# Optimization experiments

Hardware: AMD Instinct MI355X
Metric: run time of the kernel (lower is better)

The kernel has to match this reference:

```python
import jax, jax.numpy as jnp
import numpy as np

ALPHA = 0.2  # LeakyReLU negative slope
NEG_INF = -9e15


def setup_inputs() -> dict:
    key = jax.random.key(0)
    k1, k2, k3, k4 = jax.random.split(key, 4)
    B, N, F_IN, F_OUT = 2, 4096, 128, 64
    h = jax.random.normal(k1, (B, N, F_IN), dtype=jnp.float32)
    adj = jax.random.randint(k2, (N, N), 0, 2, dtype=jnp.int32)
    W = jax.random.normal(k3, (F_IN, F_OUT), dtype=jnp.float32) * (1.414 / np.sqrt(F_IN))
    a = jax.random.normal(k4, (2 * F_OUT, 1), dtype=jnp.float32) * 0.1
    return {"h": h, "adj": adj, "W": W, "a": a}


def reference(h, adj, W, a):
    # h: (B, N, F_in), adj: (N, N), W: (F_in, F_out), a: (2*F_out, 1)
    Wh = jnp.einsum("bnf,fo->bno", h, W)  # (B, N, F_out)
    F_out = W.shape[1]
    a1 = a[:F_out, 0]   # attends to source node i
    a2 = a[F_out:, 0]   # attends to target node j
    # e_ij = leakyrelu(a1.Wh_i + a2.Wh_j)  -- rank-1 decomposition of the
    # original cat([Wh_i, Wh_j]) @ a, identical math without O(N^2*2F) tensor.
    s1 = Wh @ a1  # (B, N)
    s2 = Wh @ a2  # (B, N)
    e = s1[:, :, None] + s2[:, None, :]  # (B, N, N)
    e = jnp.where(e >= 0, e, ALPHA * e)  # LeakyReLU
    scores = jnp.where(adj[None, :, :] > 0, e, NEG_INF)
    attention = jax.nn.softmax(scores, axis=-1)
    # dropout=0 (eval/deterministic baseline)
    h_prime = jnp.einsum("bij,bjo->bio", attention, Wh)  # (B, N, F_out)
    return jax.nn.elu(h_prime)  # concat=True branch
```

## Files before the change

### kernel.cpp

```cpp
#include <hip/hip_runtime.h>
#include <hip/hip_bf16.h>
#include <math.h>

#define NB 2
#define NN 4096
#define FIN 128
#define FOUT 64
#define LALPHA 0.2f

#define WS_S1    0
#define WS_S2    (NB*NN)
#define WS_WHT   (2*NB*NN)
#define WS_ABITS (WS_WHT + NB*FOUT*NN/2)


typedef __attribute__((ext_vector_type(8))) short short8;
typedef __attribute__((ext_vector_type(4))) float f32x4;

static __device__ inline unsigned int pack2bf(float x, float y) {
    float2 f2; f2.x = x; f2.y = y;
    __hip_bfloat162 pp = __float22bfloat162_rn(f2);
    return *reinterpret_cast<unsigned int*>(&pp);
}

static __device__ inline float fast_exp2(float x) {
    float r;
    asm("v_exp_f32 %0, %1" : "=v"(r) : "v"(x));
    return r;
}

#define GLL16(gsrc, ldst)                                                        \
    __builtin_amdgcn_global_load_lds(                                            \
        (const __attribute__((address_space(1))) void*)(gsrc),                   \
        (__attribute__((address_space(3))) void*)(ldst), 16, 0, 0)

__global__ __launch_bounds__(256) void k1_proj(const float* __restrict__ h,
                                               const float* __restrict__ W,
                                               const float* __restrict__ a,
                                               const int* __restrict__ adj,
                                               float* __restrict__ ws) {
    __shared__ __align__(16) float hbuf[4][128];
    __shared__ float tbuf[4][68];
    int gid  = blockIdx.x * 256 + threadIdx.x;
    int wid  = gid >> 6;
    int lane = threadIdx.x & 63;
    int w    = threadIdx.x >> 6;

    int prow = 2 * blockIdx.x + (w >> 1);
    const int4* psrc = (const int4*)(adj + (size_t)prow * NN + (w & 1) * 2048);
    int4 pv[8];
#pragma unroll
    for (int k = 0; k < 8; ++k) pv[k] = psrc[k * 64 + lane];

    const float* hrow = h + (size_t)wid * FIN;
    hbuf[w][lane]      = hrow[lane];
    hbuf[w][64 + lane] = hrow[64 + lane];

    float acc = 0.f;
#pragma unroll
    for (int f4 = 0; f4 < 32; ++f4) {
        float4 hv = *(const float4*)&hbuf[w][f4 * 4];
        acc = fmaf(hv.x, W[(f4 * 4 + 0) * FOUT + lane], acc);
        acc = fmaf(hv.y, W[(f4 * 4 + 1) * FOUT + lane], acc);
        acc = fmaf(hv.z, W[(f4 * 4 + 2) * FOUT + lane], acc);
        acc = fmaf(hv.w, W[(f4 * 4 + 3) * FOUT + lane], acc);
    }
    tbuf[w][lane] = acc;
    float v1 = acc * a[lane];
    float v2 = acc * a[FOUT + lane];
#pragma unroll
    for (int off = 32; off; off >>= 1) {
        v1 += __shfl_xor(v1, off);
        v2 += __shfl_xor(v2, off);
    }
    if (lane == 0) {
        ws[WS_S1 + wid] = v1 * 1.44269504088896f;
        ws[WS_S2 + wid] = v2 * 1.44269504088896f;
    }

    unsigned int* ab = (unsigned int*)(ws + WS_ABITS);
#pragma unroll
    for (int k = 0; k < 8; ++k) {
        unsigned int nib = (pv[k].x != 0 ? 1u : 0u)
                         | (pv[k].y != 0 ? 2u : 0u)
                         | (pv[k].z != 0 ? 4u : 0u)
                         | (pv[k].w != 0 ? 8u : 0u);
        unsigned int val = nib << ((lane & 7) * 4);
        val |= __shfl_xor(val, 1);
        val |= __shfl_xor(val, 2);
        val |= __shfl_xor(val, 4);
        if ((lane & 7) == 0)
            ab[(size_t)prow * 128 + (w & 1) * 64 + k * 8 + (lane >> 3)] = val;
    }

    __syncthreads();
    if (threadIdx.x < 64) {
        int f = threadIdx.x;
        int wid0 = blockIdx.x * 4;
        int b  = wid0 >> 12;
        int n0 = wid0 & (NN - 1);
        unsigned short* whT = (unsigned short*)(ws + WS_WHT);
        uint2 pk;
        pk.x = pack2bf(tbuf[0][f], tbuf[1][f]);
        pk.y = pack2bf(tbuf[2][f], tbuf[3][f]);
        size_t off = ((size_t)(b * 128 + (n0 >> 5)) * 2048) + f * 32 + (n0 & 31);
        *(uint2*)&whT[off] = pk;
    }
}

__global__ __launch_bounds__(1024, 4) void k3_attn(const float* __restrict__ ws,
                                                   float* __restrict__ out) {
    __shared__ float redbuf[16 * 2176];
    __shared__ float s2buf[16][256];
    __shared__ float lred[16][32];
    const int tid  = threadIdx.x;
    const int w    = tid >> 6;
    const int lane = tid & 63;
    const int col  = lane & 15;
    const int quad = lane >> 4;
    const int rt   = blockIdx.x & 127;
    const int b    = blockIdx.x >> 7;
    const int i0   = rt * 32;
    const int jbase = w * 256;

    const float* __restrict__ s1 = ws + WS_S1 + b * NN;
    const float* __restrict__ s2 = ws + WS_S2 + b * NN;
    const unsigned short* __restrict__ whT =
        (const unsigned short*)(ws + WS_WHT) + (size_t)b * FOUT * NN;
    const unsigned int* __restrict__ abits = (const unsigned int*)(ws + WS_ABITS);

    char* slot = (char*)(redbuf + w * 2176);
    float* s2s = s2buf[w];
    const unsigned short* wsrc = whT + (size_t)w * 8 * 2048;
    const int lsrc = col * 32 + quad * 8;

    unsigned int mrow[2][8];
#pragma unroll
    for (int g = 0; g < 2; ++g) {
        const int4* mp = (const int4*)&abits[(size_t)(i0 + g * 16 + col) * 128 + w * 8];
        *(int4*)&mrow[g][0] = mp[0];
        *(int4*)&mrow[g][4] = mp[1];
    }
    float s1a[2];
#pragma unroll
    for (int g = 0; g < 2; ++g) s1a[g] = s1[i0 + g * 16 + col];
    asm volatile("s_waitcnt vmcnt(0)" ::: "memory");

#define ISSUE_TILE(ks, sl)                                                \
    do {                                                                  \
        const unsigned short* wb_ = wsrc + (size_t)(ks) * 2048;           \
        GLL16(wb_ + 0 * 512 + lsrc, slot + (sl) * 4096 + 0 * 1024);       \
        GLL16(wb_ + 1 * 512 + lsrc, slot + (sl) * 4096 + 1 * 1024);       \
        GLL16(wb_ + 2 * 512 + lsrc, slot + (sl) * 4096 + 2 * 1024);       \
        GLL16(wb_ + 3 * 512 + lsrc, slot + (sl) * 4096 + 3 * 1024);       \
    } while (0)

    GLL16(&s2[jbase] + lane * 4, s2s);
    ISSUE_TILE(0, 0);
    ISSUE_TILE(1, 1);
    asm volatile("s_waitcnt vmcnt(8)" ::: "memory");

    unsigned int onew[4] = {0x3F803F80u, 0x3F803F80u, 0x3F803F80u, 0x3F803F80u};
    const short8 ones = *(short8*)onew;

    f32x4 acc[2][4];
    f32x4 accl[2];
#pragma unroll
    for (int g = 0; g < 2; ++g) {
        accl[g] = (f32x4)0.f;
#pragma unroll
        for (int nt = 0; nt < 4; ++nt) acc[g][nt] = (f32x4)0.f;
    }

#pragma unroll
    for (int ks = 0; ks < 8; ++ks) {
        const int sl = ks & 1;

        float4 s2lo = *(const float4*)&s2s[ks * 32 + quad * 8];
        float4 s2hi = *(const float4*)&s2s[ks * 32 + quad * 8 + 4];
        float sj[8] = {s2lo.x, s2lo.y, s2lo.z, s2lo.w,
                       s2hi.x, s2hi.y, s2hi.z, s2hi.w};
        short8 afrag[2];
#pragma unroll
        for (int g = 0; g < 2; ++g) {
            const unsigned int mb = (mrow[g][ks] >> (quad * 8)) & 0xffu;
            float p[8];
#pragma unroll
            for (int jj = 0; jj < 8; ++jj) {
                float e = s1a[g] + sj[jj];
                e = fmaxf(e, LALPHA * e);
                float pe = fast_exp2(e);
                p[jj] = ((mb >> jj) & 1u) ? pe : 0.f;
            }
            unsigned int pk[4];
#pragma unroll
            for (int q = 0; q < 4; ++q) pk[q] = pack2bf(p[2 * q], p[2 * q + 1]);
            afrag[g] = *(short8*)pk;
        }

        __builtin_amdgcn_sched_barrier(0);
        if (ks == 7) asm volatile("s_waitcnt vmcnt(0)" ::: "memory");
        else         asm volatile("s_waitcnt vmcnt(4)" ::: "memory");

        __builtin_amdgcn_s_setprio(1);
#pragma unroll
        for (int nt = 0; nt < 4; ++nt) {
            short8 bf = *(const short8*)(slot + sl * 4096 + nt * 1024 + lane * 16);
            acc[0][nt] = __builtin_amdgcn_mfma_f32_16x16x32_bf16(
                afrag[0], bf, acc[0][nt], 0, 0, 0);
            acc[1][nt] = __builtin_amdgcn_mfma_f32_16x16x32_bf16(
                afrag[1], bf, acc[1][nt], 0, 0, 0);
        }
        accl[0] = __builtin_amdgcn_mfma_f32_16x16x32_bf16(afrag[0], ones, accl[0], 0, 0, 0);
        accl[1] = __builtin_amdgcn_mfma_f32_16x16x32_bf16(afrag[1], ones, accl[1], 0, 0, 0);
        __builtin_amdgcn_s_setprio(0);
        if (ks < 6) ISSUE_TILE(ks + 2, sl);
    }

    float* red_w = redbuf + w * 2176;
#pragma unroll
    for (int g = 0; g < 2; ++g) {
        if (col == 0) {
#pragma unroll
            for (int reg = 0; reg < 4; ++reg)
                lred[w][g * 16 + quad * 4 + reg] = accl[g][reg];
        }
#pragma unroll
        for (int nt = 0; nt < 4; ++nt)
#pragma unroll
            for (int reg = 0; reg < 4; ++reg)
                red_w[(g * 16 + nt * 4 + reg) * 68 + lane] = acc[g][nt][reg];
    }
    __syncthreads();

#pragma unroll
    for (int e = 0; e < 2; ++e) {
        int flat = e * 1024 + tid;
        int f    = flat & 63;
        int r32  = flat >> 6;
        int g    = r32 >> 4;
        int r16  = r32 & 15;
        int q2   = r16 >> 2, reg = r16 & 3;
        int c2   = f & 15,   nt  = f >> 4;
        int ln   = q2 * 16 + c2;
        int off  = (g * 16 + nt * 4 + reg) * 68 + ln;
        float acv = 0.f, l = 0.f;
#pragma unroll
        for (int ww = 0; ww < 16; ++ww) {
            acv += redbuf[ww * 2176 + off];
            l   += lred[ww][g * 16 + r16];
        }
        float v = acv / l;
        out[((size_t)(b * NN + i0 + r32) << 6) + f] = v > 0.f ? v : (__expf(v) - 1.f);
    }
}

extern "C" void kernel_launch(void* const* d_in, const int* in_sizes, int n_in,
                              void* d_out, int out_size, void* d_ws, size_t ws_size,
                              hipStream_t stream) {
    const float* h   = (const float*)d_in[0];
    const int*   adj = (const int*)d_in[1];
    const float* W   = (const float*)d_in[2];
    const float* a   = (const float*)d_in[3];
    float* ws  = (float*)d_ws;
    float* out = (float*)d_out;

    hipLaunchKernelGGL(k1_proj, dim3(NB * NN / 4), dim3(256), 0, stream, h, W, a, adj, ws);
    hipLaunchKernelGGL(k3_attn, dim3(256), dim3(1024), 0, stream, ws, out);
}
```

Before: 123.7 us.

## Fuse projection and attention kernels via cooperative grid sync

Merges the projection/adjacency-bitpacking kernel into the attention kernel. The fused kernel computes projections, scores, bf16 transposed Wh and adjacency bits in a prologue, then synchronises the whole grid through cooperative groups before the attention phase. This is meant to remove the second kernel launch and the gap between the two kernels. In exchange it adds a grid-wide barrier and requires all 256 blocks of 1024 threads to be co-resident. It also reuses the shared-memory buffers as scratch in the prologue.

```diff
diff --git a/kernel.cpp b/kernel.cpp
--- a/kernel.cpp
+++ b/kernel.cpp
@@ -1,6 +1,9 @@
 #include <hip/hip_runtime.h>
+#include <hip/hip_cooperative_groups.h>
 #include <hip/hip_bf16.h>
 #include <math.h>
+
+namespace cg = cooperative_groups;
 
 #define NB 2
 #define NN 4096
@@ -34,95 +37,94 @@
         (const __attribute__((address_space(1))) void*)(gsrc),                   \
         (__attribute__((address_space(3))) void*)(ldst), 16, 0, 0)
 
-__global__ __launch_bounds__(256) void k1_proj(const float* __restrict__ h,
-                                               const float* __restrict__ W,
-                                               const float* __restrict__ a,
-                                               const int* __restrict__ adj,
-                                               float* __restrict__ ws) {
-    __shared__ __align__(16) float hbuf[4][128];
-    __shared__ float tbuf[4][68];
-    int gid  = blockIdx.x * 256 + threadIdx.x;
-    int wid  = gid >> 6;
-    int lane = threadIdx.x & 63;
-    int w    = threadIdx.x >> 6;
-
-    int prow = 2 * blockIdx.x + (w >> 1);
-    const int4* psrc = (const int4*)(adj + (size_t)prow * NN + (w & 1) * 2048);
-    int4 pv[8];
-#pragma unroll
-    for (int k = 0; k < 8; ++k) pv[k] = psrc[k * 64 + lane];
-
-    const float* hrow = h + (size_t)wid * FIN;
-    hbuf[w][lane]      = hrow[lane];
-    hbuf[w][64 + lane] = hrow[64 + lane];
-
-    float acc = 0.f;
-#pragma unroll
-    for (int f4 = 0; f4 < 32; ++f4) {
-        float4 hv = *(const float4*)&hbuf[w][f4 * 4];
-        acc = fmaf(hv.x, W[(f4 * 4 + 0) * FOUT + lane], acc);
-        acc = fmaf(hv.y, W[(f4 * 4 + 1) * FOUT + lane], acc);
-        acc = fmaf(hv.z, W[(f4 * 4 + 2) * FOUT + lane], acc);
-        acc = fmaf(hv.w, W[(f4 * 4 + 3) * FOUT + lane], acc);
-    }
-    tbuf[w][lane] = acc;
-    float v1 = acc * a[lane];
-    float v2 = acc * a[FOUT + lane];
-#pragma unroll
-    for (int off = 32; off; off >>= 1) {
-        v1 += __shfl_xor(v1, off);
-        v2 += __shfl_xor(v2, off);
-    }
-    if (lane == 0) {
-        ws[WS_S1 + wid] = v1 * 1.44269504088896f;
-        ws[WS_S2 + wid] = v2 * 1.44269504088896f;
-    }
-
-    unsigned int* ab = (unsigned int*)(ws + WS_ABITS);
-#pragma unroll
-    for (int k = 0; k < 8; ++k) {
-        unsigned int nib = (pv[k].x != 0 ? 1u : 0u)
-                         | (pv[k].y != 0 ? 2u : 0u)
-                         | (pv[k].z != 0 ? 4u : 0u)
-                         | (pv[k].w != 0 ? 8u : 0u);
-        unsigned int val = nib << ((lane & 7) * 4);
-        val |= __shfl_xor(val, 1);
-        val |= __shfl_xor(val, 2);
-        val |= __shfl_xor(val, 4);
-        if ((lane & 7) == 0)
-            ab[(size_t)prow * 128 + (w & 1) * 64 + k * 8 + (lane >> 3)] = val;
-    }
-
-    __syncthreads();
-    if (threadIdx.x < 64) {
-        int f = threadIdx.x;
-        int wid0 = blockIdx.x * 4;
-        int b  = wid0 >> 12;
-        int n0 = wid0 & (NN - 1);
-        unsigned short* whT = (unsigned short*)(ws + WS_WHT);
-        uint2 pk;
-        pk.x = pack2bf(tbuf[0][f], tbuf[1][f]);
-        pk.y = pack2bf(tbuf[2][f], tbuf[3][f]);
-        size_t off = ((size_t)(b * 128 + (n0 >> 5)) * 2048) + f * 32 + (n0 & 31);
-        *(uint2*)&whT[off] = pk;
-    }
-}
-
-__global__ __launch_bounds__(1024, 4) void k3_attn(const float* __restrict__ ws,
+__global__ __launch_bounds__(1024, 4) void k_fused(const float* __restrict__ h,
+                                                   const float* __restrict__ W,
+                                                   const float* __restrict__ a,
+                                                   const int* __restrict__ adj,
+                                                   float* __restrict__ ws,
                                                    float* __restrict__ out) {
-    __shared__ float redbuf[16 * 2176];
-    __shared__ float s2buf[16][256];
+    __shared__ __align__(16) float redbuf[16 * 2176];
+    __shared__ __align__(16) float s2buf[16][256];
     __shared__ float lred[16][32];
     const int tid  = threadIdx.x;
     const int w    = tid >> 6;
     const int lane = tid & 63;
     const int col  = lane & 15;
     const int quad = lane >> 4;
-    const int rt   = blockIdx.x & 127;
-    const int b    = blockIdx.x >> 7;
+    const int bid  = blockIdx.x;
+    const int rt   = bid & 127;
+    const int b    = bid >> 7;
     const int i0   = rt * 32;
+
+    {
+        const int prow = bid * 16 + w;
+        const int4* psrc = (const int4*)(adj + (size_t)prow * NN);
+        int4 pv[16];
+#pragma unroll
+        for (int k = 0; k < 16; ++k) pv[k] = psrc[k * 64 + lane];
+
+        float* hb = redbuf + w * 2176;
+        float (*tbuf)[68] = (float(*)[68])s2buf;
+        float accr[2];
+#pragma unroll
+        for (int r = 0; r < 2; ++r) {
+            const int row = i0 + 2 * w + r;
+            const float* hrow = h + (size_t)(b * NN + row) * FIN;
+            hb[lane]      = hrow[lane];
+            hb[64 + lane] = hrow[64 + lane];
+            float acc = 0.f;
+#pragma unroll
+            for (int f4 = 0; f4 < 32; ++f4) {
+                float4 hv = *(const float4*)&hb[f4 * 4];
+                acc = fmaf(hv.x, W[(f4 * 4 + 0) * FOUT + lane], acc);
+                acc = fmaf(hv.y, W[(f4 * 4 + 1) * FOUT + lane], acc);
+                acc = fmaf(hv.z, W[(f4 * 4 + 2) * FOUT + lane], acc);
+                acc = fmaf(hv.w, W[(f4 * 4 + 3) * FOUT + lane], acc);
+            }
+            accr[r] = acc;
+            float v1 = acc * a[lane];
+            float v2 = acc * a[FOUT + lane];
+#pragma unroll
+            for (int off = 32; off; off >>= 1) {
+                v1 += __shfl_xor(v1, off);
+                v2 += __shfl_xor(v2, off);
+            }
+            if (lane == 0) {
+                ws[WS_S1 + b * NN + row] = v1 * 1.44269504088896f;
+                ws[WS_S2 + b * NN + row] = v2 * 1.44269504088896f;
+            }
+        }
+        tbuf[2 * w][lane]     = accr[0];
+        tbuf[2 * w + 1][lane] = accr[1];
+
+        unsigned int* ab = (unsigned int*)(ws + WS_ABITS);
+#pragma unroll
+        for (int k = 0; k < 16; ++k) {
+            unsigned int nib = (pv[k].x != 0 ? 1u : 0u)
+                             | (pv[k].y != 0 ? 2u : 0u)
+                             | (pv[k].z != 0 ? 4u : 0u)
+                             | (pv[k].w != 0 ? 8u : 0u);
+            unsigned int val = nib << ((lane & 7) * 4);
+            val |= __shfl_xor(val, 1);
+            val |= __shfl_xor(val, 2);
+            val |= __shfl_xor(val, 4);
+            if ((lane & 7) == 0)
+                ab[(size_t)prow * 128 + k * 8 + (lane >> 3)] = val;
+        }
+
+        __syncthreads();
+        {
+            unsigned short* wt = (unsigned short*)(ws + WS_WHT) + (size_t)bid * 2048;
+            int f = tid >> 4, np = tid & 15;
+            unsigned int pk = pack2bf(tbuf[2 * np][f], tbuf[2 * np + 1][f]);
+            ((unsigned int*)wt)[f * 16 + np] = pk;
+        }
+    }
+
+    __threadfence();
+    cg::this_grid().sync();
+
     const int jbase = w * 256;
-
     const float* __restrict__ s1 = ws + WS_S1 + b * NN;
     const float* __restrict__ s2 = ws + WS_S2 + b * NN;
     const unsigned short* __restrict__ whT =
@@ -265,6 +267,7 @@
     float* ws  = (float*)d_ws;
     float* out = (float*)d_out;
 
-    hipLaunchKernelGGL(k1_proj, dim3(NB * NN / 4), dim3(256), 0, stream, h, W, a, adj, ws);
-    hipLaunchKernelGGL(k3_attn, dim3(256), dim3(1024), 0, stream, ws, out);
-}
+    void* args[] = {(void*)&h, (void*)&W, (void*)&a, (void*)&adj, (void*)&ws, (void*)&out};
+    hipLaunchCooperativeKernel(reinterpret_cast<void*>(k_fused),
+                               dim3(256), dim3(1024), args, 0, stream);
+}
```

Result: slower. 403.0 us (+225.7%).
